# Performance work log

Hardware: AMD Instinct MI355X
Metric: run time of the kernel (lower is better)

## Reference

```python
import jax, jax.numpy as jnp
import numpy as np

NUM_CHANNELS = 64
IN_FEATURES = 256
OUT_FEATURES = 256
B = 128
N = 2048


def setup_inputs() -> dict:
    key = jax.random.key(0)
    k_x, k_c, k_w, k_b = jax.random.split(key, 4)
    x = jax.random.normal(k_x, (B, N, IN_FEATURES), dtype=jnp.float32)
    channels = jax.random.randint(k_c, (N,), 0, NUM_CHANNELS, dtype=jnp.int64)
    # kaiming_uniform_(a=sqrt(5)) over fan_in -> bound = 1/sqrt(fan_in)
    wb = 1.0 / np.sqrt(IN_FEATURES)
    weight = jax.random.uniform(k_w, (NUM_CHANNELS, OUT_FEATURES, IN_FEATURES),
                                dtype=jnp.float32, minval=-wb, maxval=wb)
    bias = jax.random.uniform(k_b, (NUM_CHANNELS, OUT_FEATURES),
                              dtype=jnp.float32, minval=-wb, maxval=wb)
    return {"x": x, "channels": channels, "weight": weight, "bias": bias}


def reference(x, channels, weight, bias):
    # Gather per-point weights/biases by channel id (shared across batch).
    w = weight[channels]          # [N, out, in]
    b = bias[channels]            # [N, out]
    # Equivalent to bmm over the point axis: [B,N,in] x [N,out,in] -> [B,N,out]
    y = jnp.einsum('bni,noi->bno', x, w)
    y = y + b                     # broadcast over batch
    y = jnp.tanh(y)               # activation=True
    y = y + x                     # residual mode 1 (out == in)
    return (y, channels)
```

## Files before the change

kernel.cpp:

```cpp
#include <hip/hip_runtime.h>
#include <hip/hip_bf16.h>


#define N_SZ 2048

typedef __attribute__((ext_vector_type(8))) __bf16 bf16x8;
typedef __attribute__((ext_vector_type(4))) float  f32x4;

__device__ __forceinline__ unsigned f2bf1(float f) {
    union { float f; unsigned u; } v; v.f = f;
    return (v.u + 0x7fffu + ((v.u >> 16) & 1u)) >> 16;
}
__device__ __forceinline__ int pack2(float lo, float hi) {
    return (int)(f2bf1(lo) | (f2bf1(hi) << 16));
}
__device__ __forceinline__ float bf2f(unsigned u16) {
    union { unsigned u; float f; } v; v.u = u16 << 16;
    return v.f;
}
__device__ __forceinline__ float tanh_fast(float s) {
    float a = fabsf(s);
    float t = __expf(-2.0f * a);
    float r = (1.0f - t) * __builtin_amdgcn_rcpf(1.0f + t);
    return s < 0.0f ? -r : r;
}
__device__ __forceinline__ void gl_lds16(const void* g, void* l) {
    __builtin_amdgcn_global_load_lds(
        (const __attribute__((address_space(1))) unsigned int*)g,
        (__attribute__((address_space(3))) unsigned int*)l, 16, 0, 0);
}

__global__ __launch_bounds__(1024) void sort_kernel(const int* __restrict__ channels,
                                                    int* __restrict__ perm) {
    __shared__ int cnt[64], off[64];
    const int t = threadIdx.x;
    if (t < 64) cnt[t] = 0;
    __syncthreads();
    const int n0 = t, n1 = t + 1024;
    const int c0 = channels[n0], c1 = channels[n1];
    atomicAdd(&cnt[c0], 1);
    atomicAdd(&cnt[c1], 1);
    __syncthreads();
    if (t == 0) { int s = 0; for (int i = 0; i < 64; ++i) { off[i] = s; s += cnt[i]; } }
    __syncthreads();
    int p0 = atomicAdd(&off[c0], 1); perm[p0] = n0;
    int p1 = atomicAdd(&off[c1], 1); perm[p1] = n1;
}

__global__ __launch_bounds__(256) void wconv_kernel(const float* __restrict__ w,
                                                    unsigned char* __restrict__ wsW) {
    const int t   = blockIdx.x * 256 + threadIdx.x;
    const int c   = t >> 13;
    const int rem = t & 8191;
    const int o   = rem >> 5;
    const int ch  = rem & 31;
    const int kt  = ch >> 2;
    const int j   = ch & 3;
    const float* src = w + ((((size_t)c << 8) | o) << 8) + (ch << 3);
    float4 f0 = *(const float4*)(src);
    float4 f1 = *(const float4*)(src + 4);
    int4 p;
    p.x = pack2(f0.x, f0.y); p.y = pack2(f0.z, f0.w);
    p.z = pack2(f1.x, f1.y); p.w = pack2(f1.z, f1.w);
    const int dst = (c << 17) + (kt << 14) + ((o * 64 + j * 16) ^ ((o & 7) << 4));
    *(int4*)(wsW + dst) = p;
}

__global__ __launch_bounds__(256, 2) void channel_dense_kernel(
    const float* __restrict__ x, const int* __restrict__ channels,
    const int* __restrict__ perm, const unsigned char* __restrict__ wsW,
    const float* __restrict__ bias, float* __restrict__ y)
{
    __shared__ __align__(16) unsigned char sA[32768];
    __shared__ __align__(16) unsigned char sB[2][16384];

    const int g    = blockIdx.x;
    const int lg   = (g & 7) * 512 + (g >> 3);
    const int n    = perm[lg >> 1];
    const int half = lg & 1;
    const int tid  = threadIdx.x;
    const int c    = channels[n];
    const unsigned char* wc = wsW + ((size_t)c << 17);

    const int lane = tid & 63;
    const int wv   = tid >> 6;

    #define STAGE_W(kt, buf) do {                                              \
        const unsigned char* s_ = wc + ((kt) << 14) + (wv << 12) + (lane << 4);\
        unsigned char* d_ = sB[buf] + (wv << 12);                              \
        gl_lds16(s_,        d_);                                               \
        gl_lds16(s_ + 1024, d_ + 1024);                                        \
        gl_lds16(s_ + 2048, d_ + 2048);                                        \
        gl_lds16(s_ + 3072, d_ + 3072); } while (0)

    STAGE_W(0, 0);

    {
        const int r   = tid >> 2;
        const int sub = tid & 3;
        const float* xr = x + ((size_t)(half * 64 + r) * N_SZ + n) * 256 + sub * 64;
        const int swz = (r & 7) << 4;
        #pragma unroll
        for (int j = 0; j < 8; ++j) {
            float4 f0 = *(const float4*)(xr + j * 8);
            float4 f1 = *(const float4*)(xr + j * 8 + 4);
            int4 p;
            p.x = pack2(f0.x, f0.y); p.y = pack2(f0.z, f0.w);
            p.z = pack2(f1.x, f1.y); p.w = pack2(f1.z, f1.w);
            const int byte = (sub * 2 + (j >> 2)) * 4096 + ((r * 64 + (j & 3) * 16) ^ swz);
            *(int4*)(sA + byte) = p;
        }
    }
    __syncthreads();

    const int lr   = lane & 15;
    const int lg4  = lane >> 4;
    const int lanebyte = (lr * 64 + lg4 * 16) ^ ((lr & 7) << 4);

    f32x4 acc[4][4] = {};

    #pragma unroll
    for (int kt = 0; kt < 8; ++kt) {
        if (kt < 7) STAGE_W(kt + 1, (kt + 1) & 1);
        bf16x8 wf[4], xf[4];
        #pragma unroll
        for (int mo = 0; mo < 4; ++mo)
            wf[mo] = *(const bf16x8*)(sB[kt & 1] + (wv << 12) + (mo << 10) + lanebyte);
        #pragma unroll
        for (int nb = 0; nb < 4; ++nb)
            xf[nb] = *(const bf16x8*)(sA + (kt << 12) + (nb << 10) + lanebyte);
        #pragma unroll
        for (int mo = 0; mo < 4; ++mo)
            #pragma unroll
            for (int nb = 0; nb < 4; ++nb)
                acc[mo][nb] = __builtin_amdgcn_mfma_f32_16x16x32_bf16(wf[mo], xf[nb], acc[mo][nb], 0, 0, 0);
        __syncthreads();
    }

    const float* bch = bias + (size_t)c * 256;
    #pragma unroll
    for (int mo = 0; mo < 4; ++mo) {
        const int o0 = wv * 64 + mo * 16 + lg4 * 4;
        const float4 bv = *(const float4*)(bch + o0);
        const int kt_r  = o0 >> 5;
        const int intra = (o0 & 31) * 2;
        #pragma unroll
        for (int nb = 0; nb < 4; ++nb) {
            const int rl = nb * 16 + lr;
            const int b  = half * 64 + rl;
            const int rbyte = (kt_r << 12) + ((rl * 64 + intra) ^ ((rl & 7) << 4));
            uint2 rv = *(const uint2*)(sA + rbyte);
            float4 out;
            out.x = tanh_fast(acc[mo][nb][0] + bv.x) + bf2f(rv.x & 0xffffu);
            out.y = tanh_fast(acc[mo][nb][1] + bv.y) + bf2f(rv.x >> 16);
            out.z = tanh_fast(acc[mo][nb][2] + bv.z) + bf2f(rv.y & 0xffffu);
            out.w = tanh_fast(acc[mo][nb][3] + bv.w) + bf2f(rv.y >> 16);
            *(float4*)(y + ((size_t)b * N_SZ + n) * 256 + o0) = out;
        }
    }
    #undef STAGE_W
}

__global__ void channels_copy_kernel(const int* __restrict__ ch, float* __restrict__ out) {
    int i = blockIdx.x * 256 + threadIdx.x;
    if (i < N_SZ) out[i] = (float)ch[i];
}

extern "C" void kernel_launch(void* const* d_in, const int* in_sizes, int n_in,
                              void* d_out, int out_size, void* d_ws, size_t ws_size,
                              hipStream_t stream) {
    const float* x        = (const float*)d_in[0];
    const int*   channels = (const int*)d_in[1];
    const float* weight   = (const float*)d_in[2];
    const float* bias     = (const float*)d_in[3];
    float* y = (float*)d_out;

    unsigned char* wsW = (unsigned char*)d_ws;
    int* perm = (int*)(wsW + (64u << 17));

    sort_kernel<<<dim3(1), dim3(1024), 0, stream>>>(channels, perm);
    wconv_kernel<<<dim3(2048), dim3(256), 0, stream>>>(weight, wsW);
    channel_dense_kernel<<<dim3(4096), dim3(256), 0, stream>>>(
        x, channels, perm, wsW, bias, y);
    channels_copy_kernel<<<dim3(N_SZ / 256), dim3(256), 0, stream>>>(
        channels, y + (size_t)128 * N_SZ * 256);
}
```

Baseline: 181.5 us.

## Make dense kernel persistent per channel with register-resident weights and double-buffered x

```diff
diff --git a/kernel.cpp b/kernel.cpp
--- a/kernel.cpp
+++ b/kernel.cpp
@@ -22,16 +22,13 @@
     float a = fabsf(s);
     float t = __expf(-2.0f * a);
     float r = (1.0f - t) * __builtin_amdgcn_rcpf(1.0f + t);
-    return s < 0.0f ? -r : r;
-}
-__device__ __forceinline__ void gl_lds16(const void* g, void* l) {
-    __builtin_amdgcn_global_load_lds(
-        (const __attribute__((address_space(1))) unsigned int*)g,
-        (__attribute__((address_space(3))) unsigned int*)l, 16, 0, 0);
+    return __builtin_copysignf(r, s);
 }
 
 __global__ __launch_bounds__(1024) void sort_kernel(const int* __restrict__ channels,
-                                                    int* __restrict__ perm) {
+                                                    int* __restrict__ perm,
+                                                    int* __restrict__ start,
+                                                    float* __restrict__ out_ch) {
     __shared__ int cnt[64], off[64];
     const int t = threadIdx.x;
     if (t < 64) cnt[t] = 0;
@@ -40,130 +37,137 @@
     const int c0 = channels[n0], c1 = channels[n1];
     atomicAdd(&cnt[c0], 1);
     atomicAdd(&cnt[c1], 1);
+    out_ch[n0] = (float)c0;
+    out_ch[n1] = (float)c1;
     __syncthreads();
-    if (t == 0) { int s = 0; for (int i = 0; i < 64; ++i) { off[i] = s; s += cnt[i]; } }
+    if (t == 0) {
+        int s = 0;
+        for (int i = 0; i < 64; ++i) { start[i] = s; off[i] = s; s += cnt[i]; }
+        start[64] = s;
+    }
     __syncthreads();
     int p0 = atomicAdd(&off[c0], 1); perm[p0] = n0;
     int p1 = atomicAdd(&off[c1], 1); perm[p1] = n1;
 }
 
 __global__ __launch_bounds__(256) void wconv_kernel(const float* __restrict__ w,
-                                                    unsigned char* __restrict__ wsW) {
-    const int t   = blockIdx.x * 256 + threadIdx.x;
-    const int c   = t >> 13;
-    const int rem = t & 8191;
-    const int o   = rem >> 5;
-    const int ch  = rem & 31;
-    const int kt  = ch >> 2;
-    const int j   = ch & 3;
-    const float* src = w + ((((size_t)c << 8) | o) << 8) + (ch << 3);
+                                                    unsigned short* __restrict__ wsW) {
+    const size_t t = (size_t)blockIdx.x * 256 + threadIdx.x;
+    const float* src = w + t * 8;
     float4 f0 = *(const float4*)(src);
     float4 f1 = *(const float4*)(src + 4);
     int4 p;
     p.x = pack2(f0.x, f0.y); p.y = pack2(f0.z, f0.w);
     p.z = pack2(f1.x, f1.y); p.w = pack2(f1.z, f1.w);
-    const int dst = (c << 17) + (kt << 14) + ((o * 64 + j * 16) ^ ((o & 7) << 4));
-    *(int4*)(wsW + dst) = p;
+    *(int4*)(wsW + t * 8) = p;
 }
 
-__global__ __launch_bounds__(256, 2) void channel_dense_kernel(
-    const float* __restrict__ x, const int* __restrict__ channels,
-    const int* __restrict__ perm, const unsigned char* __restrict__ wsW,
+__global__ __launch_bounds__(512, 2) void channel_dense_kernel(
+    const float* __restrict__ x, const int* __restrict__ perm,
+    const int* __restrict__ start, const unsigned short* __restrict__ wsW,
     const float* __restrict__ bias, float* __restrict__ y)
 {
-    __shared__ __align__(16) unsigned char sA[32768];
-    __shared__ __align__(16) unsigned char sB[2][16384];
+    __shared__ __align__(16) unsigned char sA[2][65536];
 
-    const int g    = blockIdx.x;
-    const int lg   = (g & 7) * 512 + (g >> 3);
-    const int n    = perm[lg >> 1];
-    const int half = lg & 1;
+    const int c = blockIdx.x >> 2, chunk = blockIdx.x & 3;
+    const int s0 = start[c], cnt = start[c + 1] - s0;
+    const int p_begin = s0 + ((cnt * chunk) >> 2);
+    const int p_end   = s0 + ((cnt * (chunk + 1)) >> 2);
+    if (p_begin >= p_end) return;
+
     const int tid  = threadIdx.x;
-    const int c    = channels[n];
-    const unsigned char* wc = wsW + ((size_t)c << 17);
+    const int lane = tid & 63, wv = tid >> 6;
+    const int lr   = lane & 15, lg4 = lane >> 4;
 
-    const int lane = tid & 63;
-    const int wv   = tid >> 6;
-
-    #define STAGE_W(kt, buf) do {                                              \
-        const unsigned char* s_ = wc + ((kt) << 14) + (wv << 12) + (lane << 4);\
-        unsigned char* d_ = sB[buf] + (wv << 12);                              \
-        gl_lds16(s_,        d_);                                               \
-        gl_lds16(s_ + 1024, d_ + 1024);                                        \
-        gl_lds16(s_ + 2048, d_ + 2048);                                        \
-        gl_lds16(s_ + 3072, d_ + 3072); } while (0)
-
-    STAGE_W(0, 0);
-
+    bf16x8 wreg[2][8];
     {
-        const int r   = tid >> 2;
-        const int sub = tid & 3;
-        const float* xr = x + ((size_t)(half * 64 + r) * N_SZ + n) * 256 + sub * 64;
-        const int swz = (r & 7) << 4;
+        const unsigned short* wb = wsW + ((size_t)c << 16);
         #pragma unroll
-        for (int j = 0; j < 8; ++j) {
-            float4 f0 = *(const float4*)(xr + j * 8);
-            float4 f1 = *(const float4*)(xr + j * 8 + 4);
-            int4 p;
-            p.x = pack2(f0.x, f0.y); p.y = pack2(f0.z, f0.w);
-            p.z = pack2(f1.x, f1.y); p.w = pack2(f1.z, f1.w);
-            const int byte = (sub * 2 + (j >> 2)) * 4096 + ((r * 64 + (j & 3) * 16) ^ swz);
-            *(int4*)(sA + byte) = p;
+        for (int mo = 0; mo < 2; ++mo) {
+            const unsigned short* wr_ = wb + (wv * 32 + mo * 16 + lr) * 256 + lg4 * 8;
+            #pragma unroll
+            for (int kt = 0; kt < 8; ++kt)
+                wreg[mo][kt] = *(const bf16x8*)(wr_ + kt * 32);
         }
     }
+    float4 bv[2];
+    bv[0] = *(const float4*)(bias + c * 256 + wv * 32 + lg4 * 4);
+    bv[1] = *(const float4*)(bias + c * 256 + wv * 32 + 16 + lg4 * 4);
+
+    const int r  = tid >> 2;
+    const int qt = tid & 3;
+    const int wbyte = (r * 64 + qt * 16) ^ ((r & 7) << 4);
+    float4 la[8];
+
+    auto stage_load = [&](int n_, int h) {
+        const float* xb = x + ((size_t)r * N_SZ + n_) * 256 + h * 128 + qt * 8;
+        #pragma unroll
+        for (int j = 0; j < 4; ++j) {
+            la[2 * j]     = *(const float4*)(xb + j * 32);
+            la[2 * j + 1] = *(const float4*)(xb + j * 32 + 4);
+        }
+    };
+    auto stage_write = [&](int buf, int h) {
+        #pragma unroll
+        for (int j = 0; j < 4; ++j) {
+            int4 p;
+            p.x = pack2(la[2*j].x,   la[2*j].y);   p.y = pack2(la[2*j].z,   la[2*j].w);
+            p.z = pack2(la[2*j+1].x, la[2*j+1].y); p.w = pack2(la[2*j+1].z, la[2*j+1].w);
+            *(int4*)(&sA[buf][(h * 4 + j) * 8192 + wbyte]) = p;
+        }
+    };
+
+    int n_cur = perm[p_begin];
+    int n_nxt = 0;
+
+    stage_load(n_cur, 0); stage_write(0, 0);
+    stage_load(n_cur, 1); stage_write(0, 1);
     __syncthreads();
 
-    const int lr   = lane & 15;
-    const int lg4  = lane >> 4;
     const int lanebyte = (lr * 64 + lg4 * 16) ^ ((lr & 7) << 4);
 
-    f32x4 acc[4][4] = {};
+    for (int p = p_begin; p < p_end; ++p) {
+        const int cur = (p - p_begin) & 1, nxt = cur ^ 1;
+        const bool more = (p + 1 < p_end);
+        if (more) { n_nxt = perm[p + 1]; stage_load(n_nxt, 0); }
 
-    #pragma unroll
-    for (int kt = 0; kt < 8; ++kt) {
-        if (kt < 7) STAGE_W(kt + 1, (kt + 1) & 1);
-        bf16x8 wf[4], xf[4];
+        f32x4 acc[2][8] = {};
         #pragma unroll
-        for (int mo = 0; mo < 4; ++mo)
-            wf[mo] = *(const bf16x8*)(sB[kt & 1] + (wv << 12) + (mo << 10) + lanebyte);
+        for (int kt = 0; kt < 8; ++kt) {
+            bf16x8 xf[8];
+            #pragma unroll
+            for (int nb = 0; nb < 8; ++nb)
+                xf[nb] = *(const bf16x8*)(&sA[cur][kt * 8192 + nb * 1024 + lanebyte]);
+            #pragma unroll
+            for (int nb = 0; nb < 8; ++nb) {
+                acc[0][nb] = __builtin_amdgcn_mfma_f32_16x16x32_bf16(wreg[0][kt], xf[nb], acc[0][nb], 0, 0, 0);
+                acc[1][nb] = __builtin_amdgcn_mfma_f32_16x16x32_bf16(wreg[1][kt], xf[nb], acc[1][nb], 0, 0, 0);
+            }
+        }
+
+        if (more) { stage_write(nxt, 0); stage_load(n_nxt, 1); }
+
         #pragma unroll
-        for (int nb = 0; nb < 4; ++nb)
-            xf[nb] = *(const bf16x8*)(sA + (kt << 12) + (nb << 10) + lanebyte);
-        #pragma unroll
-        for (int mo = 0; mo < 4; ++mo)
+        for (int mo = 0; mo < 2; ++mo) {
+            const int o0 = wv * 32 + mo * 16 + lg4 * 4;
             #pragma unroll
-            for (int nb = 0; nb < 4; ++nb)
-                acc[mo][nb] = __builtin_amdgcn_mfma_f32_16x16x32_bf16(wf[mo], xf[nb], acc[mo][nb], 0, 0, 0);
+            for (int nb = 0; nb < 8; ++nb) {
+                const int b = nb * 16 + lr;
+                uint2 rv = *(const uint2*)(&sA[cur][wv * 8192 +
+                              ((b * 64 + mo * 32 + lg4 * 8) ^ ((lr & 7) << 4))]);
+                float4 o;
+                o.x = tanh_fast(acc[mo][nb][0] + bv[mo].x) + bf2f(rv.x & 0xffffu);
+                o.y = tanh_fast(acc[mo][nb][1] + bv[mo].y) + bf2f(rv.x >> 16);
+                o.z = tanh_fast(acc[mo][nb][2] + bv[mo].z) + bf2f(rv.y & 0xffffu);
+                o.w = tanh_fast(acc[mo][nb][3] + bv[mo].w) + bf2f(rv.y >> 16);
+                *(float4*)(y + ((size_t)b * N_SZ + n_cur) * 256 + o0) = o;
+            }
+        }
+
+        if (more) stage_write(nxt, 1);
         __syncthreads();
+        n_cur = n_nxt;
     }
-
-    const float* bch = bias + (size_t)c * 256;
-    #pragma unroll
-    for (int mo = 0; mo < 4; ++mo) {
-        const int o0 = wv * 64 + mo * 16 + lg4 * 4;
-        const float4 bv = *(const float4*)(bch + o0);
-        const int kt_r  = o0 >> 5;
-        const int intra = (o0 & 31) * 2;
-        #pragma unroll
-        for (int nb = 0; nb < 4; ++nb) {
-            const int rl = nb * 16 + lr;
-            const int b  = half * 64 + rl;
-            const int rbyte = (kt_r << 12) + ((rl * 64 + intra) ^ ((rl & 7) << 4));
-            uint2 rv = *(const uint2*)(sA + rbyte);
-            float4 out;
-            out.x = tanh_fast(acc[mo][nb][0] + bv.x) + bf2f(rv.x & 0xffffu);
-            out.y = tanh_fast(acc[mo][nb][1] + bv.y) + bf2f(rv.x >> 16);
-            out.z = tanh_fast(acc[mo][nb][2] + bv.z) + bf2f(rv.y & 0xffffu);
-            out.w = tanh_fast(acc[mo][nb][3] + bv.w) + bf2f(rv.y >> 16);
-            *(float4*)(y + ((size_t)b * N_SZ + n) * 256 + o0) = out;
-        }
-    }
-    #undef STAGE_W
-}
-
-__global__ void channels_copy_kernel(const int* __restrict__ ch, float* __restrict__ out) {
-    int i = blockIdx.x * 256 + threadIdx.x;
-    if (i < N_SZ) out[i] = (float)ch[i];
 }
 
 extern "C" void kernel_launch(void* const* d_in, const int* in_sizes, int n_in,
@@ -175,13 +179,13 @@
     const float* bias     = (const float*)d_in[3];
     float* y = (float*)d_out;
 
-    unsigned char* wsW = (unsigned char*)d_ws;
-    int* perm = (int*)(wsW + (64u << 17));
+    unsigned short* wsW = (unsigned short*)d_ws;
+    int* perm  = (int*)((unsigned char*)d_ws + (64u << 17));
+    int* start = perm + 2048;
 
-    sort_kernel<<<dim3(1), dim3(1024), 0, stream>>>(channels, perm);
+    sort_kernel<<<dim3(1), dim3(1024), 0, stream>>>(
+        channels, perm, start, y + (size_t)128 * N_SZ * 256);
     wconv_kernel<<<dim3(2048), dim3(256), 0, stream>>>(weight, wsW);
-    channel_dense_kernel<<<dim3(4096), dim3(256), 0, stream>>>(
-        x, channels, perm, wsW, bias, y);
-    channels_copy_kernel<<<dim3(N_SZ / 256), dim3(256), 0, stream>>>(
-        channels, y + (size_t)128 * N_SZ * 256);
+    channel_dense_kernel<<<dim3(256), dim3(512), 0, stream>>>(
+        x, perm, start, wsW, bias, y);
 }
```

Measured after the change: 220.6 us. +21.5%, slower.
